# Optimization experiments

Hardware: AMD Instinct MI355X
Metric: run time of the kernel (lower is better)

Reference implementation:

```python
import jax, jax.numpy as jnp
import numpy as np

B, N, DIM, H, DH = 8, 1024, 768, 12, 64
INNER = H * DH
SCALE = DH ** -0.5


def _bias_idx(n):
    # Reproduce the offset->id mapping from the torch __init__ loop:
    # offsets are first seen in row-major (p1, p2) order, so
    # id(0)=0, id(-k)=k (k=1..n-1), id(+k)=n-1+k.
    i = np.arange(n)[:, None]
    j = np.arange(n)[None, :]
    off = i - j
    idx = np.where(off <= 0, -off, n - 1 + off)
    return jnp.asarray(idx, dtype=jnp.int32)  # (n, n), values in [0, 2n-2]


def setup_inputs() -> dict:
    key = jax.random.key(0)
    ks = jax.random.split(key, 5)
    x = jax.random.normal(ks[0], (B, N, DIM), dtype=jnp.float32)
    w_qkv = jax.random.normal(ks[1], (DIM, 3 * INNER), dtype=jnp.float32) * (DIM ** -0.5)
    bias_table = jax.random.normal(ks[2], (H, 2 * N - 1), dtype=jnp.float32) * 0.02
    w_out = jax.random.normal(ks[3], (INNER, DIM), dtype=jnp.float32) * (INNER ** -0.5)
    b_out = jnp.zeros((DIM,), dtype=jnp.float32)
    bias_idx = _bias_idx(N)
    return {"x": x, "w_qkv": w_qkv, "bias_table": bias_table,
            "w_out": w_out, "b_out": b_out, "bias_idx": bias_idx}


def reference(x, w_qkv, bias_table, w_out, b_out, bias_idx):
    b, n, _ = x.shape
    qkv = x @ w_qkv  # (b, n, 3*inner)
    q, k, v = jnp.split(qkv, 3, axis=-1)
    def heads(t):
        return t.reshape(b, n, H, DH).transpose(0, 2, 1, 3)  # (b, h, n, d)
    q, k, v = heads(q), heads(k), heads(v)
    bias = bias_table[:, bias_idx]  # (h, n, n), gathered per-head relpos bias
    dots = jnp.einsum('bhid,bhjd->bhij', q, k) * SCALE + bias[None]
    attn = jax.nn.softmax(dots, axis=-1)
    out = jnp.einsum('bhij,bhjd->bhid', attn, v)
    out = out.transpose(0, 2, 1, 3).reshape(b, n, INNER)
    return out @ w_out + b_out
```

## Files before the change

### kernel.cpp

```cpp
#include <hip/hip_runtime.h>
#include <hip/hip_bf16.h>
#include <stdint.h>

typedef unsigned short u16;
typedef unsigned int u32;
typedef __bf16 bf16x8 __attribute__((ext_vector_type(8)));
typedef _Float16 f16x8 __attribute__((ext_vector_type(8)));
typedef _Float16 f16x2 __attribute__((ext_vector_type(2)));
typedef float f32x4 __attribute__((ext_vector_type(4)));
typedef unsigned short u16x4 __attribute__((ext_vector_type(4)));

#define SEQ     1024
#define DIM     768
#define NH      12
#define QKV_LD  2304
#define LOG2E   1.4426950408889634f
#define C1      0.18033688f

__device__ __forceinline__ float bf2f(u16 u) {
    union { unsigned v; float f; } x; x.v = ((unsigned)u) << 16; return x.f;
}
__device__ __forceinline__ u16 f2bf(float f) {
    union { float f; unsigned v; } x; x.f = f;
    unsigned r = (x.v + 0x7FFFu + ((x.v >> 16) & 1u)) >> 16;
    return (u16)r;
}
__device__ __forceinline__ void store_out(u16* p, float v)  { *p = f2bf(v); }
__device__ __forceinline__ void store_out(float* p, float v){ *p = v; }

__device__ __forceinline__ void async16(void* lds, const void* g) {
    __builtin_amdgcn_global_load_lds(
        (const __attribute__((address_space(1))) unsigned*)(uintptr_t)g,
        (__attribute__((address_space(3))) unsigned*)(unsigned)(uintptr_t)lds,
        16, 0, 0);
}

__global__ __launch_bounds__(256) void cvt_k(const float* __restrict__ in,
                                             u16* __restrict__ out) {
    int i = (blockIdx.x * 256 + threadIdx.x) * 4;
    float4 v = *(const float4*)(in + i);
    u16x4 o = { f2bf(v.x), f2bf(v.y), f2bf(v.z), f2bf(v.w) };
    *(u16x4*)(out + i) = o;
}

__global__ __launch_bounds__(256) void transpose_k(const float* __restrict__ in,
                                                   u16* __restrict__ out,
                                                   int R, int C) {
    __shared__ __align__(16) float t[32][33];
    int c0 = blockIdx.x * 32, r0 = blockIdx.y * 32;
    int tx = threadIdx.x & 31, ty = threadIdx.x >> 5;
#pragma unroll
    for (int i = 0; i < 32; i += 8)
        t[ty + i][tx] = in[(size_t)(r0 + ty + i) * C + c0 + tx];
    __syncthreads();
#pragma unroll
    for (int i = 0; i < 32; i += 8)
        out[(size_t)(c0 + ty + i) * R + r0 + tx] = f2bf(t[tx][ty + i]);
}

__global__ __launch_bounds__(256) void vt_k(const u16* __restrict__ qkv,
                                            _Float16* __restrict__ vT) {
    __shared__ __align__(16) u16 t[32][33];
    int bh = blockIdx.z;
    int b = bh / 12, h = bh % 12;
    int key0 = blockIdx.x * 32, dh0 = blockIdx.y * 32;
    int tx = threadIdx.x & 31, ty = threadIdx.x >> 5;
#pragma unroll
    for (int i = 0; i < 32; i += 8)
        t[ty + i][tx] = qkv[(size_t)(b * SEQ + key0 + ty + i) * QKV_LD +
                            1536 + h * 64 + dh0 + tx];
    __syncthreads();
#pragma unroll
    for (int i = 0; i < 32; i += 8)
        vT[(size_t)(bh * 64 + dh0 + ty + i) * SEQ + key0 + tx] =
            (_Float16)bf2f(t[tx][ty + i]);
}

template <int HAS_BIAS, typename OUT_T>
__global__ __launch_bounds__(256) void gemm_bt(const u16* __restrict__ A,
                                               const u16* __restrict__ Bt,
                                               const float* __restrict__ bias,
                                               OUT_T* __restrict__ C,
                                               int M, int N, int K) {
    __shared__ __align__(16) u16 sA[128 * 64];
    __shared__ __align__(16) u16 sB[128 * 64];
    const int tid = threadIdx.x;
    const int lane = tid & 63;
    const int quad = lane >> 4, l16 = lane & 15;
    const int wave = tid >> 6;
    const int m0 = blockIdx.x * 128, n0 = blockIdx.y * 128;
    const int wm = (wave >> 1) * 64, wn = (wave & 1) * 64;

    const int co0 = (quad ^ (l16 & 7)) * 8;
    f32x4 acc[4][4] = {};

    for (int k0 = 0; k0 < K; k0 += 64) {
        __syncthreads();
#pragma unroll
        for (int rep = 0; rep < 4; ++rep) {
            int i = rep * 256 + tid;
            int row = i >> 3;
            int c = (i & 7) ^ (row & 7);
            async16(&sA[i * 8], A + (size_t)(m0 + row) * K + k0 + c * 8);
            async16(&sB[i * 8], Bt + (size_t)(n0 + row) * K + k0 + c * 8);
        }
        __syncthreads();

#pragma unroll
        for (int ks = 0; ks < 2; ++ks) {
            const int co = co0 ^ (ks * 32);
            bf16x8 af[4], bfr[4];
#pragma unroll
            for (int mi = 0; mi < 4; ++mi)
                af[mi] = *(const bf16x8*)&sA[(wm + mi * 16 + l16) * 64 + co];
#pragma unroll
            for (int nj = 0; nj < 4; ++nj)
                bfr[nj] = *(const bf16x8*)&sB[(wn + nj * 16 + l16) * 64 + co];
#pragma unroll
            for (int mi = 0; mi < 4; ++mi)
#pragma unroll
                for (int nj = 0; nj < 4; ++nj)
                    acc[mi][nj] = __builtin_amdgcn_mfma_f32_16x16x32_bf16(
                        af[mi], bfr[nj], acc[mi][nj], 0, 0, 0);
        }
    }

#pragma unroll
    for (int mi = 0; mi < 4; ++mi) {
#pragma unroll
        for (int nj = 0; nj < 4; ++nj) {
            int col = n0 + wn + nj * 16 + l16;
            float bv = HAS_BIAS ? bias[col] : 0.0f;
#pragma unroll
            for (int r = 0; r < 4; ++r) {
                int row = m0 + wm + mi * 16 + quad * 4 + r;
                store_out(&C[(size_t)row * N + col], acc[mi][nj][r] + bv);
            }
        }
    }
}

__global__ __launch_bounds__(256) void attn_k(const u16* __restrict__ qkv,
                                              const _Float16* __restrict__ vT,
                                              const float* __restrict__ bias_table,
                                              u16* __restrict__ out) {
    __shared__ __align__(16) u16 sK[2][64 * 64];
    __shared__ __align__(16) _Float16 sV[2][64 * 64];
    __shared__ __align__(16) u16 sBE[2048];
    __shared__ __align__(16) _Float16 sP[4][32 * 64];

    const int tid = threadIdx.x;
    const int wave = tid >> 6, lane = tid & 63;
    const int quad = lane >> 4, l16 = lane & 15;
    const int bh = blockIdx.x;
    const int b = bh / NH, h = bh % NH;
    const int q0 = blockIdx.y * 128, wq = wave * 32;

    for (int i = tid; i < 2047; i += 256)
        sBE[i] = f2bf(LOG2E * bias_table[h * 2047 + (i <= 1023 ? 1023 - i : i)]);

    bf16x8 qf[2][2];
#pragma unroll
    for (int nt = 0; nt < 2; ++nt)
#pragma unroll
        for (int hf = 0; hf < 2; ++hf)
            qf[nt][hf] = *(const bf16x8*)(qkv +
                (size_t)(b * SEQ + q0 + wq + nt * 16 + l16) * QKV_LD +
                h * 64 + hf * 32 + quad * 8);

    const u16* kg[2];
    const _Float16* vg[2];
    int lds_i[2];
#pragma unroll
    for (int rep = 0; rep < 2; ++rep) {
        int i = rep * 256 + wave * 64 + lane;
        int row = i >> 3;
        int c = (i & 7) ^ (row & 7);
        kg[rep] = qkv + (size_t)(b * SEQ + row) * QKV_LD + 768 + h * 64 + c * 8;
        vg[rep] = vT + (size_t)(bh * 64 + row) * SEQ + c * 8;
        lds_i[rep] = i * 8;
    }

    const int co0 = (quad ^ (l16 & 7)) * 8;
    const int co1 = co0 ^ 32;
    const int par = l16 & 1;
    const int ib0 = q0 + wq + l16 - quad * 4 + 1020 - par;
    const u32 sel3 = par ? 0x03020C0Cu : 0x01000C0Cu;
    const u32 sel2 = par ? 0x05040C0Cu : 0x03020C0Cu;
    const u32 sel1 = par ? 0x07060C0Cu : 0x05040C0Cu;
    const u32 sel0 = par ? 0x05040C0Cu : 0x03020C0Cu;
    const u32* lut32 = (const u32*)sBE;

#pragma unroll
    for (int rep = 0; rep < 2; ++rep) {
        async16(&sK[0][lds_i[rep]], kg[rep]);
        async16(&sV[0][lds_i[rep]], vg[rep]);
        kg[rep] += (size_t)64 * QKV_LD;
        vg[rep] += 64;
    }
    __syncthreads();

    f32x4 o[2][4] = {};
    f32x4 osum[2] = {};
    f16x8 ones;
#pragma unroll
    for (int z = 0; z < 8; ++z) ones[z] = (_Float16)1.0f;
    _Float16* sPw = sP[wave];

    for (int kt = 0; kt < SEQ / 64; ++kt) {
        const int cur = kt & 1;
        if (kt + 1 < SEQ / 64) {
            const int nxt = cur ^ 1;
#pragma unroll
            for (int rep = 0; rep < 2; ++rep) {
                async16(&sK[nxt][lds_i[rep]], kg[rep]);
                async16(&sV[nxt][lds_i[rep]], vg[rep]);
                kg[rep] += (size_t)64 * QKV_LD;
                vg[rep] += 64;
            }
        }
        const u16* sKc = sK[cur];
        const _Float16* sVc = sV[cur];
        const int ibk = ib0 - kt * 64;

#pragma unroll
        for (int mt = 0; mt < 4; ++mt) {
            const u16* kr = sKc + mt * 1024 + l16 * 64;
            bf16x8 af0 = *(const bf16x8*)(kr + co0);
            bf16x8 af1 = *(const bf16x8*)(kr + co1);
#pragma unroll
            for (int nt = 0; nt < 2; ++nt) {
                f32x4 s = {0.f, 0.f, 0.f, 0.f};
                s = __builtin_amdgcn_mfma_f32_16x16x32_bf16(af0, qf[nt][0], s, 0, 0, 0);
                s = __builtin_amdgcn_mfma_f32_16x16x32_bf16(af1, qf[nt][1], s, 0, 0, 0);
                int w = (ibk + nt * 16 - mt * 16) >> 1;
                u32 W0 = lut32[w], W1 = lut32[w + 1], W2 = lut32[w + 2];
                float bz[4];
                bz[3] = __uint_as_float(__builtin_amdgcn_perm(W1, W0, sel3));
                bz[2] = __uint_as_float(__builtin_amdgcn_perm(W1, W0, sel2));
                bz[1] = __uint_as_float(__builtin_amdgcn_perm(W1, W0, sel1));
                bz[0] = __uint_as_float(__builtin_amdgcn_perm(W2, W1, sel0));
                float p[4];
#pragma unroll
                for (int r = 0; r < 4; ++r)
                    p[r] = __builtin_amdgcn_exp2f(fminf(s[r] * C1 + bz[r], 15.0f));
                f16x2 pk0 = __builtin_bit_cast(f16x2, __builtin_amdgcn_cvt_pkrtz(p[0], p[1]));
                f16x2 pk1 = __builtin_bit_cast(f16x2, __builtin_amdgcn_cvt_pkrtz(p[2], p[3]));
                int ch = (mt * 2 + (quad >> 1)) ^ (l16 & 7);
                _Float16* dst = &sPw[nt * 1024 + l16 * 64 + ch * 8 + (quad & 1) * 4];
                *(f16x2*)dst       = pk0;
                *(f16x2*)(dst + 2) = pk1;
            }
        }

        f16x8 pf[2][2];
#pragma unroll
        for (int mtp = 0; mtp < 2; ++mtp) {
            const _Float16* pr = sPw + mtp * 1024 + l16 * 64;
            pf[mtp][0] = *(const f16x8*)(pr + co0);
            pf[mtp][1] = *(const f16x8*)(pr + co1);
        }
#pragma unroll
        for (int mtp = 0; mtp < 2; ++mtp) {
            osum[mtp] = __builtin_amdgcn_mfma_f32_16x16x32_f16(pf[mtp][0], ones, osum[mtp], 0, 0, 0);
            osum[mtp] = __builtin_amdgcn_mfma_f32_16x16x32_f16(pf[mtp][1], ones, osum[mtp], 0, 0, 0);
        }
#pragma unroll
        for (int c4 = 0; c4 < 4; ++c4) {
            const _Float16* vr = sVc + c4 * 1024 + l16 * 64;
            f16x8 vf0 = *(const f16x8*)(vr + co0);
            f16x8 vf1 = *(const f16x8*)(vr + co1);
#pragma unroll
            for (int mtp = 0; mtp < 2; ++mtp) {
                o[mtp][c4] = __builtin_amdgcn_mfma_f32_16x16x32_f16(
                    pf[mtp][0], vf0, o[mtp][c4], 0, 0, 0);
                o[mtp][c4] = __builtin_amdgcn_mfma_f32_16x16x32_f16(
                    pf[mtp][1], vf1, o[mtp][c4], 0, 0, 0);
            }
        }
        __syncthreads();
    }

#pragma unroll
    for (int mtp = 0; mtp < 2; ++mtp) {
#pragma unroll
        for (int r = 0; r < 4; ++r) {
            float inv = __builtin_amdgcn_rcpf(osum[mtp][r]);
            int qrow = q0 + wq + mtp * 16 + quad * 4 + r;
#pragma unroll
            for (int c4 = 0; c4 < 4; ++c4)
                out[(size_t)(b * SEQ + qrow) * DIM + h * 64 + c4 * 16 + l16] =
                    f2bf(o[mtp][c4][r] * inv);
        }
    }
}

extern "C" void kernel_launch(void* const* d_in, const int* in_sizes, int n_in,
                              void* d_out, int out_size, void* d_ws, size_t ws_size,
                              hipStream_t stream) {
    const float* x          = (const float*)d_in[0];
    const float* w_qkv      = (const float*)d_in[1];
    const float* bias_table = (const float*)d_in[2];
    const float* w_out      = (const float*)d_in[3];
    const float* b_out      = (const float*)d_in[4];
    float* out = (float*)d_out;

    char* ws = (char*)d_ws;
    u16* ws_qkv        = (u16*)(ws);
    u16* ws_attn       = (u16*)(ws + 37748736);
    u16* ws_xb         = (u16*)(ws + 50331648);
    u16* ws_wqkvT      = (u16*)(ws + 62914560);
    u16* ws_woutT      = (u16*)(ws + 66453504);
    _Float16* ws_vT    = (_Float16*)(ws + 67633152);

    cvt_k<<<8 * 1024 * 768 / 1024, 256, 0, stream>>>(x, ws_xb);
    transpose_k<<<dim3(2304 / 32, 768 / 32), 256, 0, stream>>>(w_qkv, ws_wqkvT, 768, 2304);
    transpose_k<<<dim3(768 / 32, 768 / 32), 256, 0, stream>>>(w_out, ws_woutT, 768, 768);

    gemm_bt<0, u16><<<dim3(8192 / 128, 2304 / 128), 256, 0, stream>>>(
        ws_xb, ws_wqkvT, nullptr, ws_qkv, 8192, 2304, 768);

    vt_k<<<dim3(SEQ / 32, 2, 8 * NH), 256, 0, stream>>>(ws_qkv, ws_vT);

    attn_k<<<dim3(8 * NH, SEQ / 128, 1), 256, 0, stream>>>(ws_qkv, ws_vT, bias_table, ws_attn);

    gemm_bt<1, float><<<dim3(8192 / 128, 768 / 128), 256, 0, stream>>>(
        ws_attn, ws_woutT, b_out, out, 8192, 768, 768);
}
```

Before: 198.4 us.

## Keep softmax probabilities in registers and feed PV via transposed 16x16x16 MFMA

The attention kernel no longer writes the exponentiated scores to an LDS scratch tile and reads them back. It reuses the S-MFMA output layout directly as the B operand of 16x16x16 f16 MFMAs, computing O^T = V^T P^T, with row sums taken from a ones-matrix MFMA. The bias lookup table becomes an fp32 LDS array read directly, which removes the bf16 pack and perm extraction, and the fminf clamp is dropped. Outputs are now stored as 4-wide packed bf16 per row. The risks are twice as many smaller MFMAs, more V fragment loads, and possible overflow now that exp2 is unclamped.

```diff
diff --git a/kernel.cpp b/kernel.cpp
--- a/kernel.cpp
+++ b/kernel.cpp
@@ -6,9 +6,11 @@
 typedef unsigned int u32;
 typedef __bf16 bf16x8 __attribute__((ext_vector_type(8)));
 typedef _Float16 f16x8 __attribute__((ext_vector_type(8)));
-typedef _Float16 f16x2 __attribute__((ext_vector_type(2)));
+typedef _Float16 f16x4 __attribute__((ext_vector_type(4)));
+typedef __fp16 v4hf __attribute__((ext_vector_type(4)));
 typedef float f32x4 __attribute__((ext_vector_type(4)));
 typedef unsigned short u16x4 __attribute__((ext_vector_type(4)));
+typedef unsigned int u32x2 __attribute__((ext_vector_type(2)));
 
 #define SEQ     1024
 #define DIM     768
@@ -146,8 +148,7 @@
                                               u16* __restrict__ out) {
     __shared__ __align__(16) u16 sK[2][64 * 64];
     __shared__ __align__(16) _Float16 sV[2][64 * 64];
-    __shared__ __align__(16) u16 sBE[2048];
-    __shared__ __align__(16) _Float16 sP[4][32 * 64];
+    __shared__ __align__(16) float sLut[2048];
 
     const int tid = threadIdx.x;
     const int wave = tid >> 6, lane = tid & 63;
@@ -157,7 +158,7 @@
     const int q0 = blockIdx.y * 128, wq = wave * 32;
 
     for (int i = tid; i < 2047; i += 256)
-        sBE[i] = f2bf(LOG2E * bias_table[h * 2047 + (i <= 1023 ? 1023 - i : i)]);
+        sLut[i] = LOG2E * bias_table[h * 2047 + (i <= 1023 ? 1023 - i : i)];
 
     bf16x8 qf[2][2];
 #pragma unroll
@@ -183,13 +184,11 @@
 
     const int co0 = (quad ^ (l16 & 7)) * 8;
     const int co1 = co0 ^ 32;
-    const int par = l16 & 1;
-    const int ib0 = q0 + wq + l16 - quad * 4 + 1020 - par;
-    const u32 sel3 = par ? 0x03020C0Cu : 0x01000C0Cu;
-    const u32 sel2 = par ? 0x05040C0Cu : 0x03020C0Cu;
-    const u32 sel1 = par ? 0x07060C0Cu : 0x05040C0Cu;
-    const u32 sel0 = par ? 0x05040C0Cu : 0x03020C0Cu;
-    const u32* lut32 = (const u32*)sBE;
+    int voff[4];
+#pragma unroll
+    for (int mt = 0; mt < 4; ++mt)
+        voff[mt] = (((mt * 2 + (quad >> 1)) ^ (l16 & 7)) * 8) + (quad & 1) * 4;
+    const int ib0 = q0 + wq + l16 - quad * 4 + 1023;
 
 #pragma unroll
     for (int rep = 0; rep < 2; ++rep) {
@@ -202,10 +201,8 @@
 
     f32x4 o[2][4] = {};
     f32x4 osum[2] = {};
-    f16x8 ones;
-#pragma unroll
-    for (int z = 0; z < 8; ++z) ones[z] = (_Float16)1.0f;
-    _Float16* sPw = sP[wave];
+    const u32x2 onebits = { 0x3C003C00u, 0x3C003C00u };
+    const v4hf ones = __builtin_bit_cast(v4hf, onebits);
 
     for (int kt = 0; kt < SEQ / 64; ++kt) {
         const int cur = kt & 1;
@@ -223,6 +220,7 @@
         const _Float16* sVc = sV[cur];
         const int ibk = ib0 - kt * 64;
 
+        v4hf pfrag[4][2];
 #pragma unroll
         for (int mt = 0; mt < 4; ++mt) {
             const u16* kr = sKc + mt * 1024 + l16 * 64;
@@ -233,64 +231,49 @@
                 f32x4 s = {0.f, 0.f, 0.f, 0.f};
                 s = __builtin_amdgcn_mfma_f32_16x16x32_bf16(af0, qf[nt][0], s, 0, 0, 0);
                 s = __builtin_amdgcn_mfma_f32_16x16x32_bf16(af1, qf[nt][1], s, 0, 0, 0);
-                int w = (ibk + nt * 16 - mt * 16) >> 1;
-                u32 W0 = lut32[w], W1 = lut32[w + 1], W2 = lut32[w + 2];
-                float bz[4];
-                bz[3] = __uint_as_float(__builtin_amdgcn_perm(W1, W0, sel3));
-                bz[2] = __uint_as_float(__builtin_amdgcn_perm(W1, W0, sel2));
-                bz[1] = __uint_as_float(__builtin_amdgcn_perm(W1, W0, sel1));
-                bz[0] = __uint_as_float(__builtin_amdgcn_perm(W2, W1, sel0));
+                const float* bw = &sLut[ibk + nt * 16 - mt * 16];
                 float p[4];
 #pragma unroll
                 for (int r = 0; r < 4; ++r)
-                    p[r] = __builtin_amdgcn_exp2f(fminf(s[r] * C1 + bz[r], 15.0f));
-                f16x2 pk0 = __builtin_bit_cast(f16x2, __builtin_amdgcn_cvt_pkrtz(p[0], p[1]));
-                f16x2 pk1 = __builtin_bit_cast(f16x2, __builtin_amdgcn_cvt_pkrtz(p[2], p[3]));
-                int ch = (mt * 2 + (quad >> 1)) ^ (l16 & 7);
-                _Float16* dst = &sPw[nt * 1024 + l16 * 64 + ch * 8 + (quad & 1) * 4];
-                *(f16x2*)dst       = pk0;
-                *(f16x2*)(dst + 2) = pk1;
+                    p[r] = __builtin_amdgcn_exp2f(s[r] * C1 + bw[-r]);
+                u32 lo = __builtin_bit_cast(u32, __builtin_amdgcn_cvt_pkrtz(p[0], p[1]));
+                u32 hi = __builtin_bit_cast(u32, __builtin_amdgcn_cvt_pkrtz(p[2], p[3]));
+                u32x2 pk = { lo, hi };
+                pfrag[mt][nt] = __builtin_bit_cast(v4hf, pk);
             }
         }
 
-        f16x8 pf[2][2];
-#pragma unroll
-        for (int mtp = 0; mtp < 2; ++mtp) {
-            const _Float16* pr = sPw + mtp * 1024 + l16 * 64;
-            pf[mtp][0] = *(const f16x8*)(pr + co0);
-            pf[mtp][1] = *(const f16x8*)(pr + co1);
-        }
-#pragma unroll
-        for (int mtp = 0; mtp < 2; ++mtp) {
-            osum[mtp] = __builtin_amdgcn_mfma_f32_16x16x32_f16(pf[mtp][0], ones, osum[mtp], 0, 0, 0);
-            osum[mtp] = __builtin_amdgcn_mfma_f32_16x16x32_f16(pf[mtp][1], ones, osum[mtp], 0, 0, 0);
+#pragma unroll
+        for (int mt = 0; mt < 4; ++mt) {
+#pragma unroll
+            for (int nt = 0; nt < 2; ++nt)
+                osum[nt] = __builtin_amdgcn_mfma_f32_16x16x16f16(
+                    ones, pfrag[mt][nt], osum[nt], 0, 0, 0);
         }
 #pragma unroll
         for (int c4 = 0; c4 < 4; ++c4) {
-            const _Float16* vr = sVc + c4 * 1024 + l16 * 64;
-            f16x8 vf0 = *(const f16x8*)(vr + co0);
-            f16x8 vf1 = *(const f16x8*)(vr + co1);
-#pragma unroll
-            for (int mtp = 0; mtp < 2; ++mtp) {
-                o[mtp][c4] = __builtin_amdgcn_mfma_f32_16x16x32_f16(
-                    pf[mtp][0], vf0, o[mtp][c4], 0, 0, 0);
-                o[mtp][c4] = __builtin_amdgcn_mfma_f32_16x16x32_f16(
-                    pf[mtp][1], vf1, o[mtp][c4], 0, 0, 0);
+            const _Float16* vr = sVc + (c4 * 16 + l16) * 64;
+#pragma unroll
+            for (int mt = 0; mt < 4; ++mt) {
+                v4hf va = __builtin_bit_cast(v4hf, *(const f16x4*)(vr + voff[mt]));
+#pragma unroll
+                for (int nt = 0; nt < 2; ++nt)
+                    o[nt][c4] = __builtin_amdgcn_mfma_f32_16x16x16f16(
+                        va, pfrag[mt][nt], o[nt][c4], 0, 0, 0);
             }
         }
         __syncthreads();
     }
 
 #pragma unroll
-    for (int mtp = 0; mtp < 2; ++mtp) {
-#pragma unroll
-        for (int r = 0; r < 4; ++r) {
-            float inv = __builtin_amdgcn_rcpf(osum[mtp][r]);
-            int qrow = q0 + wq + mtp * 16 + quad * 4 + r;
-#pragma unroll
-            for (int c4 = 0; c4 < 4; ++c4)
-                out[(size_t)(b * SEQ + qrow) * DIM + h * 64 + c4 * 16 + l16] =
-                    f2bf(o[mtp][c4][r] * inv);
+    for (int nt = 0; nt < 2; ++nt) {
+        float inv = __builtin_amdgcn_rcpf(osum[nt][0]);
+        size_t rowbase = (size_t)(b * SEQ + q0 + wq + nt * 16 + l16) * DIM + h * 64;
+#pragma unroll
+        for (int c4 = 0; c4 < 4; ++c4) {
+            u16x4 pk = { f2bf(o[nt][c4][0] * inv), f2bf(o[nt][c4][1] * inv),
+                         f2bf(o[nt][c4][2] * inv), f2bf(o[nt][c4][3] * inv) };
+            *(u16x4*)&out[rowbase + c4 * 16 + quad * 4] = pk;
         }
     }
 }
```

New measurement: 197.9 us. About the same (-0.3%).
